# Optimization experiments

Measured on AMD Instinct MI355X. Metric: run time of the kernel, lower is better.

## Reference

```python
import jax, jax.numpy as jnp
import numpy as np

N_GRAPHS = 128
NODES_PER_GRAPH = 512
N = N_GRAPHS * NODES_PER_GRAPH  # 65536 total nodes
C = 512        # num_channels
H = 8          # num_heads
HID = C // 2   # 256


def setup_inputs() -> dict:
    key = jax.random.key(0)
    k_x, k_t, k_w1, k_w2 = jax.random.split(key, 4)
    inputs = jax.random.normal(k_x, (N, C), dtype=jnp.float32)
    n_node = jnp.full((N_GRAPHS,), NODES_PER_GRAPH, dtype=jnp.int32)  # sums to N
    task = jax.random.randint(k_t, (N_GRAPHS,), 0, H, dtype=jnp.int32)
    # lecun_normal: std = 1/sqrt(fan_in)
    W1 = jax.random.normal(k_w1, (H, C, HID), dtype=jnp.float32) / np.sqrt(C)
    b1 = jnp.zeros((H, HID), dtype=jnp.float32)
    W2 = jax.random.normal(k_w2, (H, HID, 1), dtype=jnp.float32) / np.sqrt(HID)
    b2 = jnp.zeros((H, 1), dtype=jnp.float32)
    return {"inputs": inputs, "n_node": n_node, "task": task,
            "W1": W1, "b1": b1, "W2": W2, "b2": b2}


def reference(inputs, n_node, task, W1, b1, W2, b2):
    n = inputs.shape[0]
    # per-node head id (same as repeating kernel[head] by n_node, but cheap)
    head = jnp.repeat(task, n_node, total_repeat_length=n)  # [N]
    # layer 1: grouped matmul = all-head GEMM then per-node head selection
    h_all = jnp.einsum('ni,hio->nho', inputs, W1)            # [N, H, HID]
    h = jnp.take_along_axis(h_all, head[:, None, None], axis=1)[:, 0]  # [N, HID]
    h = h + b1[head]
    h = jax.nn.silu(h)
    # layer 2: out_features == 1, so direct per-node dot with gathered weights
    y = jnp.einsum('nc,nc->n', h, W2[head, :, 0])[:, None] + b2[head]  # [N, 1]
    return y
```

## Files before the change

### kernel.cpp

```cpp
#include <hip/hip_runtime.h>
#include <hip/hip_bf16.h>
#include <stdint.h>

typedef __bf16 bf16_t;
typedef __bf16 bf16x8 __attribute__((ext_vector_type(8)));
typedef float  f32x4  __attribute__((ext_vector_type(4)));

#define NGRAPH 128
#define NPG    512
#define CIN    512
#define HID    256
#define BM     128
#define BK     64

__device__ __forceinline__ void gl2lds16(const void* g, void* l) {
  __builtin_amdgcn_global_load_lds(
      (const __attribute__((address_space(1))) uint32_t*)g,
      (__attribute__((address_space(3))) uint32_t*)l, 16, 0, 0);
}

__global__ __launch_bounds__(256) void prep_w1(const float* __restrict__ W1,
                                               bf16_t* __restrict__ Bimg) {
  __shared__ float tile[64][65];
  const int n0 = blockIdx.x * 64;
  const int kt = blockIdx.y;
  const int h  = blockIdx.z;
  const int k0 = kt * 64;
  const int tid = threadIdx.x;
  const int r = tid >> 4, c4 = tid & 15;
  const float* src = W1 + (((size_t)h * CIN + k0) * HID + n0);
#pragma unroll
  for (int i = 0; i < 4; i++) {
    const int rr = r + i * 16;
    const float4 v = *(const float4*)(src + (size_t)rr * HID + c4 * 4);
    tile[rr][c4 * 4 + 0] = v.x; tile[rr][c4 * 4 + 1] = v.y;
    tile[rr][c4 * 4 + 2] = v.z; tile[rr][c4 * 4 + 3] = v.w;
  }
  __syncthreads();
  bf16_t* dst = Bimg + (size_t)(h * 8 + kt) * 16384;
#pragma unroll
  for (int i = 0; i < 2; i++) {
    const int u = tid + i * 256;
    const int n = u >> 3, c = u & 7;
    bf16x8 o;
#pragma unroll
    for (int j = 0; j < 8; j++) o[j] = (bf16_t)tile[c * 8 + j][n];
    const int ng = n0 + n;
    const int cp = c ^ (ng & 7);
    *(bf16x8*)(dst + (size_t)ng * 64 + cp * 8) = o;
  }
}

__global__ __launch_bounds__(256, 2) void energy_main(
    const float* __restrict__ x, const int* __restrict__ task,
    const bf16_t* __restrict__ Bimg, const float* __restrict__ b1,
    const float* __restrict__ W2, const float* __restrict__ b2,
    float* __restrict__ out) {
  __shared__ float  As[BM * BK];
  __shared__ bf16_t Bs[HID * BK];
  __shared__ float  red[4][BM];

  const int bx   = blockIdx.x;
  const int g    = bx >> 2;
  const int mt   = bx & 3;
  const int head = task[g];
  const int base = g * NPG + mt * BM;
  const int tid  = threadIdx.x;
  const int wave = tid >> 6, lane = tid & 63;
  const int q = lane >> 4, t = lane & 15;

  const float*  Ag = x + (size_t)base * CIN;
  const bf16_t* Bh = Bimg + (size_t)head * 8 * 16384;

  const int a_row16 = tid >> 4;
  const int a_cp    = tid & 15;

  f32x4 acc[8][4] = {};

  for (int kt = 0; kt < 8; kt++) {
    const int k0 = kt * 64;
    if (kt) __syncthreads();
#pragma unroll
    for (int j = 0; j < 8; j++) {
      const int row = j * 16 + a_row16;
      const int c = a_cp ^ (row & 7);
      gl2lds16(Ag + (size_t)row * CIN + k0 + c * 4, As + j * 1024 + tid * 4);
    }
    const bf16_t* Bt = Bh + (size_t)kt * 16384;
#pragma unroll
    for (int j = 0; j < 8; j++)
      gl2lds16(Bt + j * 2048 + tid * 8, Bs + j * 2048 + tid * 8);
    __syncthreads();

#pragma unroll
    for (int ks = 0; ks < 64; ks += 32) {
      bf16x8 bfr[4];
#pragma unroll
      for (int ni = 0; ni < 4; ni++) {
        const int n = wave * 64 + ni * 16 + t;
        const int cp = (ks / 8 + q) ^ (n & 7);
        bfr[ni] = *(const bf16x8*)(Bs + n * 64 + cp * 8);
      }
#pragma unroll
      for (int mi = 0; mi < 8; mi++) {
        const int row = mi * 16 + t;
        const int s = row & 7;
        const int c0 = ks / 4 + q * 2;
        const float4 v0 = *(const float4*)(As + row * 64 + ((c0) ^ s) * 4);
        const float4 v1 = *(const float4*)(As + row * 64 + ((c0 + 1) ^ s) * 4);
        bf16x8 af;
        af[0] = (bf16_t)v0.x; af[1] = (bf16_t)v0.y;
        af[2] = (bf16_t)v0.z; af[3] = (bf16_t)v0.w;
        af[4] = (bf16_t)v1.x; af[5] = (bf16_t)v1.y;
        af[6] = (bf16_t)v1.z; af[7] = (bf16_t)v1.w;
#pragma unroll
        for (int ni = 0; ni < 4; ni++)
          acc[mi][ni] = __builtin_amdgcn_mfma_f32_16x16x32_bf16(
              af, bfr[ni], acc[mi][ni], 0, 0, 0);
      }
    }
  }

  float w2c[4], b1c[4];
#pragma unroll
  for (int ni = 0; ni < 4; ni++) {
    const int col = wave * 64 + ni * 16 + t;
    w2c[ni] = W2[head * HID + col];
    b1c[ni] = b1[head * HID + col];
  }
  float part[8][4];
#pragma unroll
  for (int mi = 0; mi < 8; mi++)
#pragma unroll
    for (int r = 0; r < 4; r++) {
      float sacc = 0.f;
#pragma unroll
      for (int ni = 0; ni < 4; ni++) {
        const float hh = acc[mi][ni][r] + b1c[ni];
        sacc += (hh / (1.f + __expf(-hh))) * w2c[ni];
      }
      part[mi][r] = sacc;
    }
#pragma unroll
  for (int off = 1; off < 16; off <<= 1)
#pragma unroll
    for (int mi = 0; mi < 8; mi++)
#pragma unroll
      for (int r = 0; r < 4; r++)
        part[mi][r] += __shfl_xor(part[mi][r], off, 64);
  if (t == 0) {
#pragma unroll
    for (int mi = 0; mi < 8; mi++)
#pragma unroll
      for (int r = 0; r < 4; r++)
        red[wave][mi * 16 + q * 4 + r] = part[mi][r];
  }
  __syncthreads();
  if (tid < BM) {
    out[base + tid] = red[0][tid] + red[1][tid] + red[2][tid] + red[3][tid] +
                      b2[head];
  }
}

extern "C" void kernel_launch(void* const* d_in, const int* in_sizes, int n_in,
                              void* d_out, int out_size, void* d_ws,
                              size_t ws_size, hipStream_t stream) {
  const float* x    = (const float*)d_in[0];
  const int*   task = (const int*)d_in[2];
  const float* W1   = (const float*)d_in[3];
  const float* b1   = (const float*)d_in[4];
  const float* W2   = (const float*)d_in[5];
  const float* b2   = (const float*)d_in[6];
  float* out = (float*)d_out;

  bf16_t* Bimg = (bf16_t*)d_ws;

  prep_w1<<<dim3(4, 8, 8), 256, 0, stream>>>(W1, Bimg);
  energy_main<<<dim3(NGRAPH * 4), 256, 0, stream>>>(x, task, Bimg, b1, W2, b2,
                                                    out);
}
```

Baseline: 212.7 us.

## Double-buffer LDS tiles with BK=32 to overlap loads and MFMA

Halves the K tile to 32 and allocates two LDS buffers for A and B, issuing async global-to-LDS loads for the next stage while computing the current one, with explicit vmcnt waits and barriers. The weight image layout in the prep kernel is reorganized into 16 K-slices of 32 with a new XOR swizzle to match. This aims to hide global memory latency that the previous load-sync-compute loop exposed. It doubles the number of barriers per K and relies on hand-counted vmcnt values, which could be fragile.

```diff
diff --git a/kernel.cpp b/kernel.cpp
--- a/kernel.cpp
+++ b/kernel.cpp
@@ -11,7 +11,7 @@
 #define CIN    512
 #define HID    256
 #define BM     128
-#define BK     64
+#define BK     32
 
 __device__ __forceinline__ void gl2lds16(const void* g, void* l) {
   __builtin_amdgcn_global_load_lds(
@@ -23,9 +23,9 @@
                                                bf16_t* __restrict__ Bimg) {
   __shared__ float tile[64][65];
   const int n0 = blockIdx.x * 64;
-  const int kt = blockIdx.y;
+  const int k2 = blockIdx.y;
   const int h  = blockIdx.z;
-  const int k0 = kt * 64;
+  const int k0 = k2 * 64;
   const int tid = threadIdx.x;
   const int r = tid >> 4, c4 = tid & 15;
   const float* src = W1 + (((size_t)h * CIN + k0) * HID + n0);
@@ -37,28 +37,52 @@
     tile[rr][c4 * 4 + 2] = v.z; tile[rr][c4 * 4 + 3] = v.w;
   }
   __syncthreads();
-  bf16_t* dst = Bimg + (size_t)(h * 8 + kt) * 16384;
 #pragma unroll
   for (int i = 0; i < 2; i++) {
-    const int u = tid + i * 256;
-    const int n = u >> 3, c = u & 7;
+    const int u   = tid + i * 256;
+    const int kh  = u >> 8;
+    const int rem = u & 255;
+    const int n   = rem >> 2, chp = rem & 3;
+    const int c   = chp ^ ((n >> 1) & 3);
     bf16x8 o;
 #pragma unroll
-    for (int j = 0; j < 8; j++) o[j] = (bf16_t)tile[c * 8 + j][n];
-    const int ng = n0 + n;
-    const int cp = c ^ (ng & 7);
-    *(bf16x8*)(dst + (size_t)ng * 64 + cp * 8) = o;
-  }
-}
+    for (int j = 0; j < 8; j++) o[j] = (bf16_t)tile[kh * 32 + c * 8 + j][n];
+    const int kt = k2 * 2 + kh;
+    *(bf16x8*)(Bimg + (size_t)(h * 16 + kt) * 8192 + (n0 + n) * 32 + chp * 8) = o;
+  }
+}
+
+__device__ __forceinline__ void stage_A(const float* __restrict__ Ag,
+                                        float* buf, int k0, int tid) {
+  const int ar = tid >> 3;
+  const int acp = tid & 7;
+#pragma unroll
+  for (int j = 0; j < 4; j++) {
+    const int row = j * 32 + ar;
+    const int c = acp ^ (row & 7);
+    gl2lds16(Ag + (size_t)row * CIN + k0 + c * 4, buf + j * 1024 + tid * 4);
+  }
+}
+__device__ __forceinline__ void stage_B(const bf16_t* __restrict__ Bt,
+                                        bf16_t* buf, int tid) {
+#pragma unroll
+  for (int j = 0; j < 4; j++)
+    gl2lds16(Bt + j * 2048 + tid * 8, buf + j * 2048 + tid * 8);
+}
+
+#define VMCNT8() asm volatile("s_waitcnt vmcnt(8)" ::: "memory")
+#define VMCNT0() asm volatile("s_waitcnt vmcnt(0)" ::: "memory")
+#define FENCE()  asm volatile("" ::: "memory")
+#define BAR()    __builtin_amdgcn_s_barrier()
 
 __global__ __launch_bounds__(256, 2) void energy_main(
     const float* __restrict__ x, const int* __restrict__ task,
     const bf16_t* __restrict__ Bimg, const float* __restrict__ b1,
     const float* __restrict__ W2, const float* __restrict__ b2,
     float* __restrict__ out) {
-  __shared__ float  As[BM * BK];
-  __shared__ bf16_t Bs[HID * BK];
   __shared__ float  red[4][BM];
+  __shared__ float  As0[BM * BK], As1[BM * BK];
+  __shared__ bf16_t Bs0[HID * BK], Bs1[HID * BK];
 
   const int bx   = blockIdx.x;
   const int g    = bx >> 2;
@@ -70,56 +94,58 @@
   const int q = lane >> 4, t = lane & 15;
 
   const float*  Ag = x + (size_t)base * CIN;
-  const bf16_t* Bh = Bimg + (size_t)head * 8 * 16384;
-
-  const int a_row16 = tid >> 4;
-  const int a_cp    = tid & 15;
+  const bf16_t* Bh = Bimg + (size_t)head * 16 * 8192;
 
   f32x4 acc[8][4] = {};
 
-  for (int kt = 0; kt < 8; kt++) {
-    const int k0 = kt * 64;
-    if (kt) __syncthreads();
-#pragma unroll
-    for (int j = 0; j < 8; j++) {
-      const int row = j * 16 + a_row16;
-      const int c = a_cp ^ (row & 7);
-      gl2lds16(Ag + (size_t)row * CIN + k0 + c * 4, As + j * 1024 + tid * 4);
+  auto compute = [&](const float* bA, const bf16_t* bB) {
+    bf16x8 bfr[4];
+#pragma unroll
+    for (int ni = 0; ni < 4; ni++) {
+      const int n = wave * 64 + ni * 16 + t;
+      const int sl = q ^ ((n >> 1) & 3);
+      bfr[ni] = *(const bf16x8*)(bB + n * 32 + sl * 8);
     }
-    const bf16_t* Bt = Bh + (size_t)kt * 16384;
-#pragma unroll
-    for (int j = 0; j < 8; j++)
-      gl2lds16(Bt + j * 2048 + tid * 8, Bs + j * 2048 + tid * 8);
-    __syncthreads();
-
-#pragma unroll
-    for (int ks = 0; ks < 64; ks += 32) {
-      bf16x8 bfr[4];
-#pragma unroll
-      for (int ni = 0; ni < 4; ni++) {
-        const int n = wave * 64 + ni * 16 + t;
-        const int cp = (ks / 8 + q) ^ (n & 7);
-        bfr[ni] = *(const bf16x8*)(Bs + n * 64 + cp * 8);
-      }
-#pragma unroll
-      for (int mi = 0; mi < 8; mi++) {
-        const int row = mi * 16 + t;
-        const int s = row & 7;
-        const int c0 = ks / 4 + q * 2;
-        const float4 v0 = *(const float4*)(As + row * 64 + ((c0) ^ s) * 4);
-        const float4 v1 = *(const float4*)(As + row * 64 + ((c0 + 1) ^ s) * 4);
-        bf16x8 af;
-        af[0] = (bf16_t)v0.x; af[1] = (bf16_t)v0.y;
-        af[2] = (bf16_t)v0.z; af[3] = (bf16_t)v0.w;
-        af[4] = (bf16_t)v1.x; af[5] = (bf16_t)v1.y;
-        af[6] = (bf16_t)v1.z; af[7] = (bf16_t)v1.w;
-#pragma unroll
-        for (int ni = 0; ni < 4; ni++)
-          acc[mi][ni] = __builtin_amdgcn_mfma_f32_16x16x32_bf16(
-              af, bfr[ni], acc[mi][ni], 0, 0, 0);
-      }
+#pragma unroll
+    for (int mi = 0; mi < 8; mi++) {
+      const int row = mi * 16 + t;
+      const int s = row & 7;
+      const float4 v0 = *(const float4*)(bA + row * 32 + ((2 * q) ^ s) * 4);
+      const float4 v1 = *(const float4*)(bA + row * 32 + ((2 * q + 1) ^ s) * 4);
+      bf16x8 af;
+      af[0] = (bf16_t)v0.x; af[1] = (bf16_t)v0.y;
+      af[2] = (bf16_t)v0.z; af[3] = (bf16_t)v0.w;
+      af[4] = (bf16_t)v1.x; af[5] = (bf16_t)v1.y;
+      af[6] = (bf16_t)v1.z; af[7] = (bf16_t)v1.w;
+#pragma unroll
+      for (int ni = 0; ni < 4; ni++)
+        acc[mi][ni] = __builtin_amdgcn_mfma_f32_16x16x32_bf16(
+            af, bfr[ni], acc[mi][ni], 0, 0, 0);
     }
-  }
+  };
+
+  stage_A(Ag, As0, 0, tid);  stage_B(Bh, Bs0, tid);
+  stage_A(Ag, As1, BK, tid); stage_B(Bh + 8192, Bs1, tid);
+
+  for (int kt = 0; kt < 14; kt += 2) {
+    VMCNT8();
+    BAR();
+    compute(As0, Bs0);
+    FENCE(); BAR();
+    stage_A(Ag, As0, (kt + 2) * BK, tid);
+    stage_B(Bh + (size_t)(kt + 2) * 8192, Bs0, tid);
+
+    VMCNT8();
+    BAR();
+    compute(As1, Bs1);
+    FENCE(); BAR();
+    stage_A(Ag, As1, (kt + 3) * BK, tid);
+    stage_B(Bh + (size_t)(kt + 3) * 8192, Bs1, tid);
+  }
+  VMCNT8(); BAR();
+  compute(As0, Bs0);
+  VMCNT0(); BAR();
+  compute(As1, Bs1);
 
   float w2c[4], b1c[4];
 #pragma unroll
```

Measured after the change: 214.1 us. Within noise of the previous version (+0.6%).
